# Kernel optimization log

Hardware: AMD Instinct MI355X
Metric: run time of the kernel (lower is better)

Reference implementation:

```python
import jax, jax.numpy as jnp
import numpy as np

B, T, C, H, E, K = 4, 2048, 512, 2048, 8, 2


def setup_inputs() -> dict:
    key = jax.random.key(0)
    ks = jax.random.split(key, 7)
    s_r = 1.0 / np.sqrt(C)
    s_h = 1.0 / np.sqrt(H)
    return {
        "x": jax.random.normal(ks[0], (B, T, C), dtype=jnp.float32),
        "Wr": jax.random.uniform(ks[1], (C, E), jnp.float32, -s_r, s_r),
        "br": jax.random.uniform(ks[2], (E,), jnp.float32, -s_r, s_r),
        "W1": jax.random.uniform(ks[3], (E, C, H), jnp.float32, -s_r, s_r),
        "b1": jax.random.uniform(ks[4], (E, H), jnp.float32, -s_r, s_r),
        "W2": jax.random.uniform(ks[5], (E, H, C), jnp.float32, -s_h, s_h),
        "b2": jax.random.uniform(ks[6], (E, C), jnp.float32, -s_h, s_h),
    }


def reference(x, Wr, br, W1, b1, W2, b2):
    # Router logits [B,T,E]
    logits = jnp.einsum("btc,ce->bte", x, Wr) + br
    topk_vals, topk_idx = jax.lax.top_k(logits, K)  # [B,T,K]
    scores = jax.nn.softmax(topk_vals, axis=-1)  # softmax over the K selected
    # Combine weights per expert: gate[b,t,e] = sum_k scores[b,t,k]*(idx==e)
    onehot = jax.nn.one_hot(topk_idx, E, dtype=x.dtype)  # [B,T,K,E]
    gate = jnp.einsum("btk,btke->bte", scores, onehot)  # [B,T,E]
    # Dense-masked expert MLPs (tokens not routed to e have gate==0)
    h = jax.nn.relu(jnp.einsum("btc,ech->bteh", x, W1) + b1)  # [B,T,E,H]
    y = jnp.einsum("bteh,ehc->btec", h, W2) + b2  # [B,T,E,C]
    out = jnp.einsum("btec,bte->btc", y, gate)  # weighted combine
    return logits, topk_idx, out
```

## Files before the change

### kernel.cpp

```cpp
#include <hip/hip_runtime.h>
#include <hip/hip_bf16.h>

#define NTOK 8192
#define NASN 16384
#define C_ 512
#define H_ 2048
#define E_ 8
#define NCH 128
#define CHTOK 64

typedef __bf16 bf16x8 __attribute__((ext_vector_type(8)));
typedef float f32x4 __attribute__((ext_vector_type(4)));

#define WS_COUNTS 0
#define WS_BASE   4096
#define WS_OFFS   8192
#define WS_T1S    8448
#define WS_INFO   8704
#define WS_TOKL   (WS_INFO + NTOK*16)
#define WS_SLOTS  (WS_TOKL + NASN*4)
#define WS_XBF    (WS_SLOTS + NTOK*8)
#define WS_W1B    (WS_XBF + (size_t)NTOK*C_*2)
#define WS_W2B    (WS_W1B + (size_t)E_*H_*C_*2)
#define WS_HS     (WS_W2B + (size_t)E_*H_*C_*2)
#define WS_YS     WS_XBF

__device__ __forceinline__ unsigned int f2bf(float f) {
  __hip_bfloat16 h = __float2bfloat16(f);
  return (unsigned int)*(unsigned short*)&h;
}
__device__ __forceinline__ float bf2f(unsigned int u) {
  return __int_as_float((u & 0xffffu) << 16);
}

__device__ __forceinline__ void g2l16(const unsigned short* g, unsigned short* l) {
  __builtin_amdgcn_global_load_lds(
      (const __attribute__((address_space(1))) unsigned int*)g,
      (__attribute__((address_space(3))) unsigned int*)l, 16, 0, 0);
}

__global__ __launch_bounds__(256) void k_router(
    const float* __restrict__ x, const float* __restrict__ Wr,
    const float* __restrict__ br, float* __restrict__ out_logits,
    float* __restrict__ out_idx, int4* __restrict__ info,
    int* __restrict__ counts, unsigned short* __restrict__ Xbf)
{
  int t = blockIdx.x * 4 + (threadIdx.x >> 6);
  int lane = threadIdx.x & 63;
  const float4* xr = (const float4*)(x + (size_t)t * C_);
  float4 x0 = xr[lane*2], x1 = xr[lane*2+1];
  uint4 pk;
  pk.x = f2bf(x0.x) | (f2bf(x0.y) << 16);
  pk.y = f2bf(x0.z) | (f2bf(x0.w) << 16);
  pk.z = f2bf(x1.x) | (f2bf(x1.y) << 16);
  pk.w = f2bf(x1.z) | (f2bf(x1.w) << 16);
  *(uint4*)(Xbf + (size_t)t * C_ + lane*8) = pk;

  float xs[8] = {x0.x,x0.y,x0.z,x0.w,x1.x,x1.y,x1.z,x1.w};
  float acc[8] = {0,0,0,0,0,0,0,0};
  #pragma unroll
  for (int j = 0; j < 8; j++) {
    const float4* w = (const float4*)(Wr + (size_t)(lane*8+j) * E_);
    float4 w0 = w[0], w1 = w[1];
    float we[8] = {w0.x,w0.y,w0.z,w0.w,w1.x,w1.y,w1.z,w1.w};
    #pragma unroll
    for (int e = 0; e < 8; e++) acc[e] += xs[j] * we[e];
  }
  #pragma unroll
  for (int off = 1; off < 64; off <<= 1) {
    #pragma unroll
    for (int e = 0; e < 8; e++) acc[e] += __shfl_xor(acc[e], off, 64);
  }
  #pragma unroll
  for (int e = 0; e < 8; e++) acc[e] += br[e];
  if (lane == 0) {
    #pragma unroll
    for (int e = 0; e < 8; e++) out_logits[t*8 + e] = acc[e];
    int i0 = 0; float v0 = acc[0];
    #pragma unroll
    for (int e = 1; e < 8; e++) if (acc[e] > v0) { v0 = acc[e]; i0 = e; }
    int i1 = -1; float v1 = -1e30f;
    #pragma unroll
    for (int e = 0; e < 8; e++) if (e != i0 && acc[e] > v1) { v1 = acc[e]; i1 = e; }
    float d = expf(v1 - v0);
    float s1 = d / (1.0f + d);
    float s0 = 1.0f - s1;
    out_idx[t*2]     = (float)i0;
    out_idx[t*2 + 1] = (float)i1;
    info[t] = make_int4(i0, i1, __float_as_int(s0), __float_as_int(s1));
    int ch = t >> 6;
    atomicAdd(&counts[ch*8 + i0], 1);
    atomicAdd(&counts[ch*8 + i1], 1);
  }
}

__global__ __launch_bounds__(256) void k_prefix(
    const int* __restrict__ counts, int* __restrict__ base,
    int* __restrict__ offs, int* __restrict__ t1s)
{
  __shared__ int lc[NCH*8];
  __shared__ int tot[8];
  __shared__ int off_s[9];
  int tid = threadIdx.x;
  for (int i = tid; i < NCH*8; i += 256) lc[i] = counts[i];
  __syncthreads();
  if (tid < 8) {
    int run = 0;
    for (int c = 0; c < NCH; c++) { int v = lc[c*8+tid]; lc[c*8+tid] = run; run += v; }
    tot[tid] = run;
  }
  __syncthreads();
  if (tid == 0) {
    int o = 0, t = 0;
    off_s[0] = 0; offs[0] = 0; t1s[0] = 0;
    for (int e = 0; e < 8; e++) {
      o += tot[e];
      off_s[e+1] = o; offs[e+1] = o;
      t += (tot[e] + 127) >> 7;
      t1s[e+1] = t;
    }
  }
  __syncthreads();
  for (int i = tid; i < NCH*8; i += 256) base[i] = off_s[i & 7] + lc[i];
}

__global__ __launch_bounds__(64) void k_scatter(
    const int4* __restrict__ info, const int* __restrict__ base,
    int* __restrict__ tokl, int2* __restrict__ slots2)
{
  __shared__ int cur[8];
  int c = blockIdx.x, tid = threadIdx.x;
  if (tid < 8) cur[tid] = base[c*8 + tid];
  __syncthreads();
  int t = c * CHTOK + tid;
  int4 nfo = info[t];
  int r0 = atomicAdd(&cur[nfo.x], 1);
  int r1 = atomicAdd(&cur[nfo.y], 1);
  tokl[r0] = t;
  tokl[r1] = t;
  slots2[t] = make_int2(r0, r1);
}

__global__ __launch_bounds__(256) void k_transpose(
    const float* __restrict__ in, unsigned short* __restrict__ outp, int R, int S)
{
  __shared__ float tile[128][33];
  size_t zo = (size_t)blockIdx.z * R * S;
  in += zo; outp += zo;
  int r0 = blockIdx.y * 128, s0 = blockIdx.x * 32;
  int t = threadIdx.x;
  #pragma unroll
  for (int i = 0; i < 16; i++) {
    int lin = i*256 + t;
    int rr = lin >> 5, ss = lin & 31;
    tile[rr][ss] = in[(size_t)(r0 + rr) * S + s0 + ss];
  }
  __syncthreads();
  #pragma unroll
  for (int i = 0; i < 4; i++) {
    int lin = i*256 + t;
    int ss = lin >> 5, rq = lin & 31;
    ushort4 v;
    v.x = (unsigned short)f2bf(tile[rq*4+0][ss]);
    v.y = (unsigned short)f2bf(tile[rq*4+1][ss]);
    v.z = (unsigned short)f2bf(tile[rq*4+2][ss]);
    v.w = (unsigned short)f2bf(tile[rq*4+3][ss]);
    *(ushort4*)(outp + (size_t)(s0 + ss) * R + r0 + rq*4) = v;
  }
}

__global__ __launch_bounds__(256) void k_gemm1(
    const unsigned short* __restrict__ Xbf, const int* __restrict__ tokl,
    const unsigned short* __restrict__ W1b,
    const float* __restrict__ b1, unsigned short* __restrict__ Hs,
    const int* __restrict__ offs, const int* __restrict__ t1s)
{
  __shared__ __align__(16) unsigned short AB[2*8192];
  int b = blockIdx.x;
  int mo = b >> 7, rr = b & 127;
  int n0 = (rr >> 3) * 128;
  int mt = mo*8 + (rr & 7);
  if (mt >= t1s[8]) return;
  int e = 0;
  #pragma unroll
  for (int i = 0; i < 7; i++) if (mt >= t1s[e+1]) e++;
  int row0 = offs[e] + (mt - t1s[e]) * 128;
  int rowEnd = offs[e+1];
  int tid = threadIdx.x, lane = tid & 63, w = tid >> 6;
  int wm = (w & 1) * 64, wn = (w >> 1) * 64;
  int quad = lane >> 4, l16 = lane & 15;
  const f32x4 zero = {0.f, 0.f, 0.f, 0.f};
  f32x4 acc[4][4];
  #pragma unroll
  for (int i = 0; i < 4; i++)
    #pragma unroll
    for (int j = 0; j < 4; j++) acc[i][j] = zero;
  const unsigned short* Bsrc = W1b + ((size_t)e * H_ + n0) * C_;

  const unsigned short* ga[2]; const unsigned short* gb[2];
  int lao[2], lbo[2];
  #pragma unroll
  for (int j = 0; j < 2; j++) {
    int L = (w*2 + j)*64 + lane;
    int row = L >> 2;
    int gc = (L & 3) ^ (row & 3);
    int gr = row0 + row; gr = gr < NASN-1 ? gr : NASN-1;
    int trow = tokl[gr];
    ga[j] = Xbf + (size_t)trow * C_ + gc*8;
    gb[j] = Bsrc + (size_t)row * C_ + gc*8;
    lao[j] = (w*2 + j)*512;
    lbo[j] = 4096 + (w*2 + j)*512;
  }
  int r3 = l16 & 3;
  const int KI = C_ / 32;

  #pragma unroll
  for (int j = 0; j < 2; j++) { g2l16(ga[j], AB + lao[j]); g2l16(gb[j], AB + lbo[j]); }

  for (int ki = 0; ki < KI; ki++) {
    int p = ki & 1;
    if (ki + 1 < KI) {
      int off = (ki + 1) * 32;
      unsigned short* nb = AB + (p ^ 1) * 8192;
      #pragma unroll
      for (int j = 0; j < 2; j++) {
        g2l16(ga[j] + off, nb + lao[j]);
        g2l16(gb[j] + off, nb + lbo[j]);
      }
      asm volatile("s_waitcnt vmcnt(4)" ::: "memory");
    } else {
      asm volatile("s_waitcnt vmcnt(0)" ::: "memory");
    }
    asm volatile("s_barrier" ::: "memory");

    const unsigned short* Ap = AB + p*8192;
    const unsigned short* Bp = Ap + 4096;
    int sl = (quad ^ r3) * 8;
    bf16x8 af[4], bfr[4];
    #pragma unroll
    for (int i = 0; i < 4; i++)
      af[i] = *(const bf16x8*)&Ap[(wm + i*16 + l16)*32 + sl];
    #pragma unroll
    for (int j = 0; j < 4; j++)
      bfr[j] = *(const bf16x8*)&Bp[(wn + j*16 + l16)*32 + sl];
    #pragma unroll
    for (int i = 0; i < 4; i++)
      #pragma unroll
      for (int j = 0; j < 4; j++)
        acc[i][j] = __builtin_amdgcn_mfma_f32_16x16x32_bf16(af[i], bfr[j], acc[i][j], 0, 0, 0);

    asm volatile("s_waitcnt lgkmcnt(0)" ::: "memory");
    asm volatile("s_barrier" ::: "memory");
  }

  unsigned short* Lt = AB + w*4096;
  #pragma unroll
  for (int j = 0; j < 4; j++) {
    int n = n0 + wn + j*16 + l16;
    float bias = b1[e * H_ + n];
    #pragma unroll
    for (int i = 0; i < 4; i++)
      #pragma unroll
      for (int r = 0; r < 4; r++) {
        float v = acc[i][j][r] + bias;
        Lt[(i*16 + quad*4 + r)*64 + j*16 + l16] = (unsigned short)f2bf(v > 0.f ? v : 0.f);
      }
  }
  #pragma unroll
  for (int it = 0; it < 8; it++) {
    int rloc = it*8 + (lane >> 3);
    int m = row0 + wm + rloc;
    uint4 vv = *(uint4*)&Lt[rloc*64 + (lane & 7)*8];
    if (m < rowEnd)
      *(uint4*)(Hs + (size_t)m * H_ + n0 + wn + (lane & 7)*8) = vv;
  }
}

__global__ __launch_bounds__(256) void k_gemm2(
    const unsigned short* __restrict__ Hs, const unsigned short* __restrict__ W2b,
    const float* __restrict__ b2, unsigned short* __restrict__ Ys,
    const int* __restrict__ offs, const int* __restrict__ t1s)
{
  __shared__ __align__(16) unsigned short AB[2*8192];
  int b = blockIdx.x;
  int g = b >> 5, rr = b & 31;
  int n0 = (rr >> 3) * 128;
  int mt = g*8 + (rr & 7);
  if (mt >= t1s[8]) return;
  int e = 0;
  #pragma unroll
  for (int i = 0; i < 7; i++) if (mt >= t1s[e+1]) e++;
  int row0 = offs[e] + (mt - t1s[e]) * 128;
  int rowEnd = offs[e+1];
  int tid = threadIdx.x, lane = tid & 63, w = tid >> 6;
  int wm = (w & 1) * 64, wn = (w >> 1) * 64;
  int quad = lane >> 4, l16 = lane & 15;
  const f32x4 zero = {0.f, 0.f, 0.f, 0.f};
  f32x4 acc[4][4];
  #pragma unroll
  for (int i = 0; i < 4; i++)
    #pragma unroll
    for (int j = 0; j < 4; j++) acc[i][j] = zero;
  const unsigned short* Bsrc = W2b + ((size_t)e * C_ + n0) * H_;

  const unsigned short* ga[2]; const unsigned short* gb[2];
  int lao[2], lbo[2];
  #pragma unroll
  for (int j = 0; j < 2; j++) {
    int L = (w*2 + j)*64 + lane;
    int row = L >> 2;
    int gc = (L & 3) ^ (row & 3);
    int gr = row0 + row; gr = gr < NASN-1 ? gr : NASN-1;
    ga[j] = Hs + (size_t)gr * H_ + gc*8;
    gb[j] = Bsrc + (size_t)row * H_ + gc*8;
    lao[j] = (w*2 + j)*512;
    lbo[j] = 4096 + (w*2 + j)*512;
  }
  int r3 = l16 & 3;
  const int KI = H_ / 32;

  #pragma unroll
  for (int j = 0; j < 2; j++) { g2l16(ga[j], AB + lao[j]); g2l16(gb[j], AB + lbo[j]); }

  for (int ki = 0; ki < KI; ki++) {
    int p = ki & 1;
    if (ki + 1 < KI) {
      int off = (ki + 1) * 32;
      unsigned short* nb = AB + (p ^ 1) * 8192;
      #pragma unroll
      for (int j = 0; j < 2; j++) {
        g2l16(ga[j] + off, nb + lao[j]);
        g2l16(gb[j] + off, nb + lbo[j]);
      }
      asm volatile("s_waitcnt vmcnt(4)" ::: "memory");
    } else {
      asm volatile("s_waitcnt vmcnt(0)" ::: "memory");
    }
    asm volatile("s_barrier" ::: "memory");

    const unsigned short* Ap = AB + p*8192;
    const unsigned short* Bp = Ap + 4096;
    int sl = (quad ^ r3) * 8;
    bf16x8 af[4], bfr[4];
    #pragma unroll
    for (int i = 0; i < 4; i++)
      af[i] = *(const bf16x8*)&Ap[(wm + i*16 + l16)*32 + sl];
    #pragma unroll
    for (int j = 0; j < 4; j++)
      bfr[j] = *(const bf16x8*)&Bp[(wn + j*16 + l16)*32 + sl];
    #pragma unroll
    for (int i = 0; i < 4; i++)
      #pragma unroll
      for (int j = 0; j < 4; j++)
        acc[i][j] = __builtin_amdgcn_mfma_f32_16x16x32_bf16(af[i], bfr[j], acc[i][j], 0, 0, 0);

    asm volatile("s_waitcnt lgkmcnt(0)" ::: "memory");
    asm volatile("s_barrier" ::: "memory");
  }

  unsigned short* Lt = AB + w*4096;
  #pragma unroll
  for (int j = 0; j < 4; j++) {
    int n = n0 + wn + j*16 + l16;
    float bias = b2[e * C_ + n];
    #pragma unroll
    for (int i = 0; i < 4; i++)
      #pragma unroll
      for (int r = 0; r < 4; r++)
        Lt[(i*16 + quad*4 + r)*64 + j*16 + l16] =
            (unsigned short)f2bf(acc[i][j][r] + bias);
  }
  #pragma unroll
  for (int it = 0; it < 8; it++) {
    int rloc = it*8 + (lane >> 3);
    int m = row0 + wm + rloc;
    uint4 vv = *(uint4*)&Lt[rloc*64 + (lane & 7)*8];
    if (m < rowEnd)
      *(uint4*)(Ys + (size_t)m * C_ + n0 + wn + (lane & 7)*8) = vv;
  }
}

__global__ __launch_bounds__(256) void k_combine(
    const unsigned short* __restrict__ Ys, const int4* __restrict__ info,
    const int2* __restrict__ slots2, float* __restrict__ outp)
{
  int t = blockIdx.x * 4 + (threadIdx.x >> 6);
  int lane = threadIdx.x & 63;
  int4 nfo = info[t];
  int2 ss = slots2[t];
  float g0 = __int_as_float(nfo.z), g1 = __int_as_float(nfo.w);
  uint4 a = *(const uint4*)(Ys + (size_t)ss.x * C_ + lane*8);
  uint4 bb = *(const uint4*)(Ys + (size_t)ss.y * C_ + lane*8);
  unsigned int au[4] = {a.x, a.y, a.z, a.w};
  unsigned int bu[4] = {bb.x, bb.y, bb.z, bb.w};
  float vals[8];
  #pragma unroll
  for (int q = 0; q < 4; q++) {
    vals[q*2]   = g0*bf2f(au[q])       + g1*bf2f(bu[q]);
    vals[q*2+1] = g0*bf2f(au[q] >> 16) + g1*bf2f(bu[q] >> 16);
  }
  float4 o0, o1;
  o0.x = vals[0]; o0.y = vals[1]; o0.z = vals[2]; o0.w = vals[3];
  o1.x = vals[4]; o1.y = vals[5]; o1.z = vals[6]; o1.w = vals[7];
  float4* o = (float4*)(outp + (size_t)t * C_ + lane*8);
  o[0] = o0;
  o[1] = o1;
}

extern "C" void kernel_launch(void* const* d_in, const int* in_sizes, int n_in,
                              void* d_out, int out_size, void* d_ws, size_t ws_size,
                              hipStream_t stream)
{
  const float* x  = (const float*)d_in[0];
  const float* Wr = (const float*)d_in[1];
  const float* br = (const float*)d_in[2];
  const float* W1 = (const float*)d_in[3];
  const float* b1 = (const float*)d_in[4];
  const float* W2 = (const float*)d_in[5];
  const float* b2 = (const float*)d_in[6];
  float* out = (float*)d_out;
  char* ws = (char*)d_ws;

  int*  counts = (int*)(ws + WS_COUNTS);
  int*  base   = (int*)(ws + WS_BASE);
  int*  offs   = (int*)(ws + WS_OFFS);
  int*  t1s    = (int*)(ws + WS_T1S);
  int4* info   = (int4*)(ws + WS_INFO);
  int*  tokl   = (int*)(ws + WS_TOKL);
  int2* slots2 = (int2*)(ws + WS_SLOTS);
  unsigned short* Xbf = (unsigned short*)(ws + WS_XBF);
  unsigned short* W1b = (unsigned short*)(ws + WS_W1B);
  unsigned short* W2b = (unsigned short*)(ws + WS_W2B);
  unsigned short* Hs  = (unsigned short*)(ws + WS_HS);
  unsigned short* Ys  = (unsigned short*)(ws + WS_YS);

  hipMemsetAsync(counts, 0, NCH*8*sizeof(int), stream);

  k_transpose<<<dim3(H_/32, C_/128, E_), 256, 0, stream>>>(W1, W1b, C_, H_);
  k_transpose<<<dim3(C_/32, H_/128, E_), 256, 0, stream>>>(W2, W2b, H_, C_);
  k_router<<<NTOK/4, 256, 0, stream>>>(x, Wr, br, out, out + 65536, info, counts, Xbf);
  k_prefix<<<1, 256, 0, stream>>>(counts, base, offs, t1s);
  k_scatter<<<NCH, 64, 0, stream>>>(info, base, tokl, slots2);
  k_gemm1<<<17*128, 256, 0, stream>>>(Xbf, tokl, W1b, b1, Hs, offs, t1s);
  k_gemm2<<<17*32, 256, 0, stream>>>(Hs, W2b, b2, Ys, offs, t1s);
  k_combine<<<NTOK/4, 256, 0, stream>>>(Ys, info, slots2, out + 81920);
}
```

Before: 279.6 us.

## Halve gemm2 M-tile to 64 rows and change LDS swizzle layout for both GEMMs

The second expert GEMM now uses 64-row M tiles instead of 128, with a separate tile-prefix array (t2s) and about twice as many blocks. The intent is better CU occupancy and load balance for the small N=512 output, where gemm2 previously launched only about 544 blocks. Both GEMMs also switch to a new LDS staging layout that pairs two rows per 64-element line with an XOR swizzle, meant to reduce LDS bank conflicts on fragment reads. The smaller tile lowers data reuse per block and re-reads W2 more often.

```diff
diff --git a/kernel.cpp b/kernel.cpp
--- a/kernel.cpp
+++ b/kernel.cpp
@@ -16,7 +16,8 @@
 #define WS_BASE   4096
 #define WS_OFFS   8192
 #define WS_T1S    8448
-#define WS_INFO   8704
+#define WS_T2S    8704
+#define WS_INFO   8960
 #define WS_TOKL   (WS_INFO + NTOK*16)
 #define WS_SLOTS  (WS_TOKL + NASN*4)
 #define WS_XBF    (WS_SLOTS + NTOK*8)
@@ -37,6 +38,13 @@
   __builtin_amdgcn_global_load_lds(
       (const __attribute__((address_space(1))) unsigned int*)g,
       (__attribute__((address_space(3))) unsigned int*)l, 16, 0, 0);
+}
+
+__device__ __forceinline__ void stage_decode(int L, int& brow, int& q) {
+  int s = L >> 3, slot = L & 7;
+  int v = slot ^ (s & 7);
+  brow = 2*s + (v >> 2);
+  q = v & 3;
 }
 
 __global__ __launch_bounds__(256) void k_router(
@@ -96,7 +104,7 @@
 
 __global__ __launch_bounds__(256) void k_prefix(
     const int* __restrict__ counts, int* __restrict__ base,
-    int* __restrict__ offs, int* __restrict__ t1s)
+    int* __restrict__ offs, int* __restrict__ t1s, int* __restrict__ t2s)
 {
   __shared__ int lc[NCH*8];
   __shared__ int tot[8];
@@ -111,13 +119,15 @@
   }
   __syncthreads();
   if (tid == 0) {
-    int o = 0, t = 0;
-    off_s[0] = 0; offs[0] = 0; t1s[0] = 0;
+    int o = 0, t1 = 0, t2 = 0;
+    off_s[0] = 0; offs[0] = 0; t1s[0] = 0; t2s[0] = 0;
     for (int e = 0; e < 8; e++) {
       o += tot[e];
       off_s[e+1] = o; offs[e+1] = o;
-      t += (tot[e] + 127) >> 7;
-      t1s[e+1] = t;
+      t1 += (tot[e] + 127) >> 7;
+      t1s[e+1] = t1;
+      t2 += (tot[e] + 63) >> 6;
+      t2s[e+1] = t2;
     }
   }
   __syncthreads();
@@ -202,16 +212,15 @@
   #pragma unroll
   for (int j = 0; j < 2; j++) {
     int L = (w*2 + j)*64 + lane;
-    int row = L >> 2;
-    int gc = (L & 3) ^ (row & 3);
-    int gr = row0 + row; gr = gr < NASN-1 ? gr : NASN-1;
+    int brow, q; stage_decode(L, brow, q);
+    int gr = row0 + brow; gr = gr < NASN-1 ? gr : NASN-1;
     int trow = tokl[gr];
-    ga[j] = Xbf + (size_t)trow * C_ + gc*8;
-    gb[j] = Bsrc + (size_t)row * C_ + gc*8;
+    ga[j] = Xbf + (size_t)trow * C_ + q*8;
+    gb[j] = Bsrc + (size_t)brow * C_ + q*8;
     lao[j] = (w*2 + j)*512;
     lbo[j] = 4096 + (w*2 + j)*512;
   }
-  int r3 = l16 & 3;
+  int rbase = (l16>>1)*64 + ((((l16&1)<<2) + quad) ^ (l16>>1))*8;
   const int KI = C_ / 32;
 
   #pragma unroll
@@ -235,14 +244,13 @@
 
     const unsigned short* Ap = AB + p*8192;
     const unsigned short* Bp = Ap + 4096;
-    int sl = (quad ^ r3) * 8;
     bf16x8 af[4], bfr[4];
     #pragma unroll
     for (int i = 0; i < 4; i++)
-      af[i] = *(const bf16x8*)&Ap[(wm + i*16 + l16)*32 + sl];
+      af[i] = *(const bf16x8*)&Ap[wm*32 + i*512 + rbase];
     #pragma unroll
     for (int j = 0; j < 4; j++)
-      bfr[j] = *(const bf16x8*)&Bp[(wn + j*16 + l16)*32 + sl];
+      bfr[j] = *(const bf16x8*)&Bp[wn*32 + j*512 + rbase];
     #pragma unroll
     for (int i = 0; i < 4; i++)
       #pragma unroll
@@ -279,77 +287,78 @@
 __global__ __launch_bounds__(256) void k_gemm2(
     const unsigned short* __restrict__ Hs, const unsigned short* __restrict__ W2b,
     const float* __restrict__ b2, unsigned short* __restrict__ Ys,
-    const int* __restrict__ offs, const int* __restrict__ t1s)
-{
-  __shared__ __align__(16) unsigned short AB[2*8192];
+    const int* __restrict__ offs, const int* __restrict__ t2s)
+{
+  __shared__ __align__(16) unsigned short AB[2*6144];
   int b = blockIdx.x;
-  int g = b >> 5, rr = b & 31;
+  int mo = b >> 5, rr = b & 31;
   int n0 = (rr >> 3) * 128;
-  int mt = g*8 + (rr & 7);
-  if (mt >= t1s[8]) return;
+  int mt = mo*8 + (rr & 7);
+  if (mt >= t2s[8]) return;
   int e = 0;
   #pragma unroll
-  for (int i = 0; i < 7; i++) if (mt >= t1s[e+1]) e++;
-  int row0 = offs[e] + (mt - t1s[e]) * 128;
+  for (int i = 0; i < 7; i++) if (mt >= t2s[e+1]) e++;
+  int row0 = offs[e] + (mt - t2s[e]) * 64;
   int rowEnd = offs[e+1];
   int tid = threadIdx.x, lane = tid & 63, w = tid >> 6;
-  int wm = (w & 1) * 64, wn = (w >> 1) * 64;
+  int wm = (w & 1) * 32, wn = (w >> 1) * 64;
   int quad = lane >> 4, l16 = lane & 15;
   const f32x4 zero = {0.f, 0.f, 0.f, 0.f};
-  f32x4 acc[4][4];
-  #pragma unroll
-  for (int i = 0; i < 4; i++)
+  f32x4 acc[2][4];
+  #pragma unroll
+  for (int i = 0; i < 2; i++)
     #pragma unroll
     for (int j = 0; j < 4; j++) acc[i][j] = zero;
   const unsigned short* Bsrc = W2b + ((size_t)e * C_ + n0) * H_;
 
-  const unsigned short* ga[2]; const unsigned short* gb[2];
-  int lao[2], lbo[2];
+  const unsigned short* gA; int laoA;
+  const unsigned short* gb[2]; int lbo[2];
+  {
+    int L = w*64 + lane;
+    int brow, q; stage_decode(L, brow, q);
+    int gr = row0 + brow; gr = gr < NASN-1 ? gr : NASN-1;
+    gA = Hs + (size_t)gr * H_ + q*8;
+    laoA = w*512;
+  }
   #pragma unroll
   for (int j = 0; j < 2; j++) {
     int L = (w*2 + j)*64 + lane;
-    int row = L >> 2;
-    int gc = (L & 3) ^ (row & 3);
-    int gr = row0 + row; gr = gr < NASN-1 ? gr : NASN-1;
-    ga[j] = Hs + (size_t)gr * H_ + gc*8;
-    gb[j] = Bsrc + (size_t)row * H_ + gc*8;
-    lao[j] = (w*2 + j)*512;
-    lbo[j] = 4096 + (w*2 + j)*512;
-  }
-  int r3 = l16 & 3;
+    int brow, q; stage_decode(L, brow, q);
+    gb[j] = Bsrc + (size_t)brow * H_ + q*8;
+    lbo[j] = 2048 + (w*2 + j)*512;
+  }
+  int rbase = (l16>>1)*64 + ((((l16&1)<<2) + quad) ^ (l16>>1))*8;
   const int KI = H_ / 32;
 
-  #pragma unroll
-  for (int j = 0; j < 2; j++) { g2l16(ga[j], AB + lao[j]); g2l16(gb[j], AB + lbo[j]); }
+  g2l16(gA, AB + laoA);
+  #pragma unroll
+  for (int j = 0; j < 2; j++) g2l16(gb[j], AB + lbo[j]);
 
   for (int ki = 0; ki < KI; ki++) {
     int p = ki & 1;
     if (ki + 1 < KI) {
       int off = (ki + 1) * 32;
-      unsigned short* nb = AB + (p ^ 1) * 8192;
-      #pragma unroll
-      for (int j = 0; j < 2; j++) {
-        g2l16(ga[j] + off, nb + lao[j]);
-        g2l16(gb[j] + off, nb + lbo[j]);
-      }
-      asm volatile("s_waitcnt vmcnt(4)" ::: "memory");
+      unsigned short* nb = AB + (p ^ 1) * 6144;
+      g2l16(gA + off, nb + laoA);
+      #pragma unroll
+      for (int j = 0; j < 2; j++) g2l16(gb[j] + off, nb + lbo[j]);
+      asm volatile("s_waitcnt vmcnt(3)" ::: "memory");
     } else {
       asm volatile("s_waitcnt vmcnt(0)" ::: "memory");
     }
     asm volatile("s_barrier" ::: "memory");
 
-    const unsigned short* Ap = AB + p*8192;
-    const unsigned short* Bp = Ap + 4096;
-    int sl = (quad ^ r3) * 8;
-    bf16x8 af[4], bfr[4];
-    #pragma unroll
-    for (int i = 0; i < 4; i++)
-      af[i] = *(const bf16x8*)&Ap[(wm + i*16 + l16)*32 + sl];
+    const unsigned short* Ap = AB + p*6144;
+    const unsigned short* Bp = Ap + 2048;
+    bf16x8 af[2], bfr[4];
+    #pragma unroll
+    for (int i = 0; i < 2; i++)
+      af[i] = *(const bf16x8*)&Ap[wm*32 + i*512 + rbase];
     #pragma unroll
     for (int j = 0; j < 4; j++)
-      bfr[j] = *(const bf16x8*)&Bp[(wn + j*16 + l16)*32 + sl];
-    #pragma unroll
-    for (int i = 0; i < 4; i++)
+      bfr[j] = *(const bf16x8*)&Bp[wn*32 + j*512 + rbase];
+    #pragma unroll
+    for (int i = 0; i < 2; i++)
       #pragma unroll
       for (int j = 0; j < 4; j++)
         acc[i][j] = __builtin_amdgcn_mfma_f32_16x16x32_bf16(af[i], bfr[j], acc[i][j], 0, 0, 0);
@@ -358,20 +367,20 @@
     asm volatile("s_barrier" ::: "memory");
   }
 
-  unsigned short* Lt = AB + w*4096;
+  unsigned short* Lt = AB + w*2048;
   #pragma unroll
   for (int j = 0; j < 4; j++) {
     int n = n0 + wn + j*16 + l16;
     float bias = b2[e * C_ + n];
     #pragma unroll
-    for (int i = 0; i < 4; i++)
+    for (int i = 0; i < 2; i++)
       #pragma unroll
       for (int r = 0; r < 4; r++)
         Lt[(i*16 + quad*4 + r)*64 + j*16 + l16] =
             (unsigned short)f2bf(acc[i][j][r] + bias);
   }
   #pragma unroll
-  for (int it = 0; it < 8; it++) {
+  for (int it = 0; it < 4; it++) {
     int rloc = it*8 + (lane >> 3);
     int m = row0 + wm + rloc;
     uint4 vv = *(uint4*)&Lt[rloc*64 + (lane & 7)*8];
@@ -425,6 +434,7 @@
   int*  base   = (int*)(ws + WS_BASE);
   int*  offs   = (int*)(ws + WS_OFFS);
   int*  t1s    = (int*)(ws + WS_T1S);
+  int*  t2s    = (int*)(ws + WS_T2S);
   int4* info   = (int4*)(ws + WS_INFO);
   int*  tokl   = (int*)(ws + WS_TOKL);
   int2* slots2 = (int2*)(ws + WS_SLOTS);
@@ -439,9 +449,9 @@
   k_transpose<<<dim3(H_/32, C_/128, E_), 256, 0, stream>>>(W1, W1b, C_, H_);
   k_transpose<<<dim3(C_/32, H_/128, E_), 256, 0, stream>>>(W2, W2b, H_, C_);
   k_router<<<NTOK/4, 256, 0, stream>>>(x, Wr, br, out, out + 65536, info, counts, Xbf);
-  k_prefix<<<1, 256, 0, stream>>>(counts, base, offs, t1s);
+  k_prefix<<<1, 256, 0, stream>>>(counts, base, offs, t1s, t2s);
   k_scatter<<<NCH, 64, 0, stream>>>(info, base, tokl, slots2);
   k_gemm1<<<17*128, 256, 0, stream>>>(Xbf, tokl, W1b, b1, Hs, offs, t1s);
-  k_gemm2<<<17*32, 256, 0, stream>>>(Hs, W2b, b2, Ys, offs, t1s);
+  k_gemm2<<<33*32, 256, 0, stream>>>(Hs, W2b, b2, Ys, offs, t2s);
   k_combine<<<NTOK/4, 256, 0, stream>>>(Ys, info, slots2, out + 81920);
 }
```

After: 285.4 us. 2.1% more time.

## Fuse router with weight transposes, merge prefix into scatter, rework LDS swizzle

Applied to the files above, without the earlier changes.

Router and both weight-transpose kernels now run as one launch, partitioned by block index. Per-block expert counts are written with plain stores instead of global atomics, which removes the memset. Prefix and scatter are merged so each scatter block recomputes its own base offsets from the per-block counts. This cuts four launches and a memset down to two. The GEMM staging layout also changes to an 8-slot XOR swizzle over pairs of rows, meant to reduce LDS bank conflicts on fragment reads. The cost is that every scatter block re-reads all 16K count entries.

```diff
diff --git a/kernel.cpp b/kernel.cpp
--- a/kernel.cpp
+++ b/kernel.cpp
@@ -6,17 +6,15 @@
 #define C_ 512
 #define H_ 2048
 #define E_ 8
-#define NCH 128
-#define CHTOK 64
+#define RBC 2048
 
 typedef __bf16 bf16x8 __attribute__((ext_vector_type(8)));
 typedef float f32x4 __attribute__((ext_vector_type(4)));
 
 #define WS_COUNTS 0
-#define WS_BASE   4096
-#define WS_OFFS   8192
-#define WS_T1S    8448
-#define WS_INFO   8704
+#define WS_OFFS   65536
+#define WS_T1S    65792
+#define WS_INFO   66048
 #define WS_TOKL   (WS_INFO + NTOK*16)
 #define WS_SLOTS  (WS_TOKL + NASN*4)
 #define WS_XBF    (WS_SLOTS + NTOK*8)
@@ -39,134 +37,173 @@
       (__attribute__((address_space(3))) unsigned int*)l, 16, 0, 0);
 }
 
-__global__ __launch_bounds__(256) void k_router(
+__device__ __forceinline__ void stage_decode(int L, int& brow, int& q) {
+  int s = L >> 3, slot = L & 7;
+  int v = slot ^ (s & 7);
+  brow = 2*s + (v >> 2);
+  q = v & 3;
+}
+
+__global__ __launch_bounds__(256) void k_fused(
     const float* __restrict__ x, const float* __restrict__ Wr,
     const float* __restrict__ br, float* __restrict__ out_logits,
     float* __restrict__ out_idx, int4* __restrict__ info,
-    int* __restrict__ counts, unsigned short* __restrict__ Xbf)
-{
-  int t = blockIdx.x * 4 + (threadIdx.x >> 6);
-  int lane = threadIdx.x & 63;
-  const float4* xr = (const float4*)(x + (size_t)t * C_);
-  float4 x0 = xr[lane*2], x1 = xr[lane*2+1];
-  uint4 pk;
-  pk.x = f2bf(x0.x) | (f2bf(x0.y) << 16);
-  pk.y = f2bf(x0.z) | (f2bf(x0.w) << 16);
-  pk.z = f2bf(x1.x) | (f2bf(x1.y) << 16);
-  pk.w = f2bf(x1.z) | (f2bf(x1.w) << 16);
-  *(uint4*)(Xbf + (size_t)t * C_ + lane*8) = pk;
-
-  float xs[8] = {x0.x,x0.y,x0.z,x0.w,x1.x,x1.y,x1.z,x1.w};
-  float acc[8] = {0,0,0,0,0,0,0,0};
-  #pragma unroll
-  for (int j = 0; j < 8; j++) {
-    const float4* w = (const float4*)(Wr + (size_t)(lane*8+j) * E_);
-    float4 w0 = w[0], w1 = w[1];
-    float we[8] = {w0.x,w0.y,w0.z,w0.w,w1.x,w1.y,w1.z,w1.w};
-    #pragma unroll
-    for (int e = 0; e < 8; e++) acc[e] += xs[j] * we[e];
-  }
-  #pragma unroll
-  for (int off = 1; off < 64; off <<= 1) {
-    #pragma unroll
-    for (int e = 0; e < 8; e++) acc[e] += __shfl_xor(acc[e], off, 64);
-  }
-  #pragma unroll
-  for (int e = 0; e < 8; e++) acc[e] += br[e];
-  if (lane == 0) {
-    #pragma unroll
-    for (int e = 0; e < 8; e++) out_logits[t*8 + e] = acc[e];
-    int i0 = 0; float v0 = acc[0];
-    #pragma unroll
-    for (int e = 1; e < 8; e++) if (acc[e] > v0) { v0 = acc[e]; i0 = e; }
-    int i1 = -1; float v1 = -1e30f;
-    #pragma unroll
-    for (int e = 0; e < 8; e++) if (e != i0 && acc[e] > v1) { v1 = acc[e]; i1 = e; }
-    float d = expf(v1 - v0);
-    float s1 = d / (1.0f + d);
-    float s0 = 1.0f - s1;
-    out_idx[t*2]     = (float)i0;
-    out_idx[t*2 + 1] = (float)i1;
-    info[t] = make_int4(i0, i1, __float_as_int(s0), __float_as_int(s1));
-    int ch = t >> 6;
-    atomicAdd(&counts[ch*8 + i0], 1);
-    atomicAdd(&counts[ch*8 + i1], 1);
-  }
-}
-
-__global__ __launch_bounds__(256) void k_prefix(
-    const int* __restrict__ counts, int* __restrict__ base,
+    int* __restrict__ counts, unsigned short* __restrict__ Xbf,
+    const float* __restrict__ W1, unsigned short* __restrict__ W1b,
+    const float* __restrict__ W2, unsigned short* __restrict__ W2b)
+{
+  __shared__ float tileS[128][33];
+  __shared__ int bc[8];
+  int b = blockIdx.x;
+  int tid = threadIdx.x;
+
+  if (b < RBC) {
+    if (tid < 8) bc[tid] = 0;
+    __syncthreads();
+    int t = b * 4 + (tid >> 6);
+    int lane = tid & 63;
+    const float4* xr = (const float4*)(x + (size_t)t * C_);
+    float4 x0 = xr[lane*2], x1 = xr[lane*2+1];
+    uint4 pk;
+    pk.x = f2bf(x0.x) | (f2bf(x0.y) << 16);
+    pk.y = f2bf(x0.z) | (f2bf(x0.w) << 16);
+    pk.z = f2bf(x1.x) | (f2bf(x1.y) << 16);
+    pk.w = f2bf(x1.z) | (f2bf(x1.w) << 16);
+    *(uint4*)(Xbf + (size_t)t * C_ + lane*8) = pk;
+
+    float xs[8] = {x0.x,x0.y,x0.z,x0.w,x1.x,x1.y,x1.z,x1.w};
+    float acc[8] = {0,0,0,0,0,0,0,0};
+    #pragma unroll
+    for (int j = 0; j < 8; j++) {
+      const float4* w = (const float4*)(Wr + (size_t)(lane*8+j) * E_);
+      float4 w0 = w[0], w1 = w[1];
+      float we[8] = {w0.x,w0.y,w0.z,w0.w,w1.x,w1.y,w1.z,w1.w};
+      #pragma unroll
+      for (int e = 0; e < 8; e++) acc[e] += xs[j] * we[e];
+    }
+    #pragma unroll
+    for (int off = 1; off < 64; off <<= 1) {
+      #pragma unroll
+      for (int e = 0; e < 8; e++) acc[e] += __shfl_xor(acc[e], off, 64);
+    }
+    #pragma unroll
+    for (int e = 0; e < 8; e++) acc[e] += br[e];
+    if (lane == 0) {
+      #pragma unroll
+      for (int e = 0; e < 8; e++) out_logits[t*8 + e] = acc[e];
+      int i0 = 0; float v0 = acc[0];
+      #pragma unroll
+      for (int e = 1; e < 8; e++) if (acc[e] > v0) { v0 = acc[e]; i0 = e; }
+      int i1 = -1; float v1 = -1e30f;
+      #pragma unroll
+      for (int e = 0; e < 8; e++) if (e != i0 && acc[e] > v1) { v1 = acc[e]; i1 = e; }
+      float d = expf(v1 - v0);
+      float s1 = d / (1.0f + d);
+      float s0 = 1.0f - s1;
+      out_idx[t*2]     = (float)i0;
+      out_idx[t*2 + 1] = (float)i1;
+      info[t] = make_int4(i0, i1, __float_as_int(s0), __float_as_int(s1));
+      atomicAdd(&bc[i0], 1);
+      atomicAdd(&bc[i1], 1);
+    }
+    __syncthreads();
+    if (tid < 8) counts[b*8 + tid] = bc[tid];
+    return;
+  }
+
+  const float* in; unsigned short* outp; int R, S, bx, by, bz;
+  if (b < 2*RBC) {
+    int bb = b - RBC;
+    in = W1; outp = W1b; R = C_; S = H_;
+    bx = bb & 63; by = (bb >> 6) & 3; bz = bb >> 8;
+  } else {
+    int bb = b - 2*RBC;
+    in = W2; outp = W2b; R = H_; S = C_;
+    bx = bb & 15; by = (bb >> 4) & 15; bz = bb >> 8;
+  }
+  size_t zo = (size_t)bz * R * S;
+  in += zo; outp += zo;
+  int r0 = by * 128, s0 = bx * 32;
+  #pragma unroll
+  for (int i = 0; i < 16; i++) {
+    int lin = i*256 + tid;
+    int rr = lin >> 5, ss = lin & 31;
+    tileS[rr][ss] = in[(size_t)(r0 + rr) * S + s0 + ss];
+  }
+  __syncthreads();
+  #pragma unroll
+  for (int i = 0; i < 4; i++) {
+    int lin = i*256 + tid;
+    int ss = lin >> 5, rq = lin & 31;
+    ushort4 v;
+    v.x = (unsigned short)f2bf(tileS[rq*4+0][ss]);
+    v.y = (unsigned short)f2bf(tileS[rq*4+1][ss]);
+    v.z = (unsigned short)f2bf(tileS[rq*4+2][ss]);
+    v.w = (unsigned short)f2bf(tileS[rq*4+3][ss]);
+    *(ushort4*)(outp + (size_t)(s0 + ss) * R + r0 + rq*4) = v;
+  }
+}
+
+__global__ __launch_bounds__(64) void k_prefscatter(
+    const int* __restrict__ counts, const int4* __restrict__ info,
+    int* __restrict__ tokl, int2* __restrict__ slots2,
     int* __restrict__ offs, int* __restrict__ t1s)
 {
-  __shared__ int lc[NCH*8];
-  __shared__ int tot[8];
+  __shared__ int full_s[8][8];
+  __shared__ int part_s[8][8];
+  __shared__ int tot_s[8];
   __shared__ int off_s[9];
-  int tid = threadIdx.x;
-  for (int i = tid; i < NCH*8; i += 256) lc[i] = counts[i];
+  __shared__ int cur[8];
+  int c = blockIdx.x, t = threadIdx.x;
+  int e = t & 7, g = t >> 3;
+  int lim = c * 16;
+  int full = 0, part = 0;
+  for (int i = 0; i < 256; i++) {
+    int rb = g*256 + i;
+    int v = counts[rb*8 + e];
+    full += v;
+    if (rb < lim) part += v;
+  }
+  full_s[e][g] = full; part_s[e][g] = part;
   __syncthreads();
-  if (tid < 8) {
-    int run = 0;
-    for (int c = 0; c < NCH; c++) { int v = lc[c*8+tid]; lc[c*8+tid] = run; run += v; }
-    tot[tid] = run;
+  if (t < 8) {
+    int s = 0;
+    #pragma unroll
+    for (int gg = 0; gg < 8; gg++) s += full_s[t][gg];
+    tot_s[t] = s;
   }
   __syncthreads();
-  if (tid == 0) {
-    int o = 0, t = 0;
-    off_s[0] = 0; offs[0] = 0; t1s[0] = 0;
-    for (int e = 0; e < 8; e++) {
-      o += tot[e];
-      off_s[e+1] = o; offs[e+1] = o;
-      t += (tot[e] + 127) >> 7;
-      t1s[e+1] = t;
+  if (t == 0) {
+    int o = 0;
+    off_s[0] = 0;
+    for (int ee = 0; ee < 8; ee++) { o += tot_s[ee]; off_s[ee+1] = o; }
+    if (c == 0) {
+      offs[0] = 0; t1s[0] = 0;
+      int tt = 0;
+      for (int ee = 0; ee < 8; ee++) {
+        offs[ee+1] = off_s[ee+1];
+        tt += (tot_s[ee] + 127) >> 7;
+        t1s[ee+1] = tt;
+      }
     }
   }
   __syncthreads();
-  for (int i = tid; i < NCH*8; i += 256) base[i] = off_s[i & 7] + lc[i];
-}
-
-__global__ __launch_bounds__(64) void k_scatter(
-    const int4* __restrict__ info, const int* __restrict__ base,
-    int* __restrict__ tokl, int2* __restrict__ slots2)
-{
-  __shared__ int cur[8];
-  int c = blockIdx.x, tid = threadIdx.x;
-  if (tid < 8) cur[tid] = base[c*8 + tid];
+  if (t < 8) {
+    int mg = c >> 4;
+    int bse = off_s[t];
+    #pragma unroll
+    for (int gg = 0; gg < 8; gg++) if (gg < mg) bse += full_s[t][gg];
+    bse += part_s[t][mg];
+    cur[t] = bse;
+  }
   __syncthreads();
-  int t = c * CHTOK + tid;
-  int4 nfo = info[t];
+  int tok = c*64 + t;
+  int4 nfo = info[tok];
   int r0 = atomicAdd(&cur[nfo.x], 1);
   int r1 = atomicAdd(&cur[nfo.y], 1);
-  tokl[r0] = t;
-  tokl[r1] = t;
-  slots2[t] = make_int2(r0, r1);
-}
-
-__global__ __launch_bounds__(256) void k_transpose(
-    const float* __restrict__ in, unsigned short* __restrict__ outp, int R, int S)
-{
-  __shared__ float tile[128][33];
-  size_t zo = (size_t)blockIdx.z * R * S;
-  in += zo; outp += zo;
-  int r0 = blockIdx.y * 128, s0 = blockIdx.x * 32;
-  int t = threadIdx.x;
-  #pragma unroll
-  for (int i = 0; i < 16; i++) {
-    int lin = i*256 + t;
-    int rr = lin >> 5, ss = lin & 31;
-    tile[rr][ss] = in[(size_t)(r0 + rr) * S + s0 + ss];
-  }
-  __syncthreads();
-  #pragma unroll
-  for (int i = 0; i < 4; i++) {
-    int lin = i*256 + t;
-    int ss = lin >> 5, rq = lin & 31;
-    ushort4 v;
-    v.x = (unsigned short)f2bf(tile[rq*4+0][ss]);
-    v.y = (unsigned short)f2bf(tile[rq*4+1][ss]);
-    v.z = (unsigned short)f2bf(tile[rq*4+2][ss]);
-    v.w = (unsigned short)f2bf(tile[rq*4+3][ss]);
-    *(ushort4*)(outp + (size_t)(s0 + ss) * R + r0 + rq*4) = v;
-  }
+  tokl[r0] = tok;
+  tokl[r1] = tok;
+  slots2[tok] = make_int2(r0, r1);
 }
 
 __global__ __launch_bounds__(256) void k_gemm1(
@@ -202,16 +239,15 @@
   #pragma unroll
   for (int j = 0; j < 2; j++) {
     int L = (w*2 + j)*64 + lane;
-    int row = L >> 2;
-    int gc = (L & 3) ^ (row & 3);
-    int gr = row0 + row; gr = gr < NASN-1 ? gr : NASN-1;
+    int brow, q; stage_decode(L, brow, q);
+    int gr = row0 + brow; gr = gr < NASN-1 ? gr : NASN-1;
     int trow = tokl[gr];
-    ga[j] = Xbf + (size_t)trow * C_ + gc*8;
-    gb[j] = Bsrc + (size_t)row * C_ + gc*8;
+    ga[j] = Xbf + (size_t)trow * C_ + q*8;
+    gb[j] = Bsrc + (size_t)brow * C_ + q*8;
     lao[j] = (w*2 + j)*512;
     lbo[j] = 4096 + (w*2 + j)*512;
   }
-  int r3 = l16 & 3;
+  int rbase = (l16>>1)*64 + ((((l16&1)<<2) + quad) ^ (l16>>1))*8;
   const int KI = C_ / 32;
 
   #pragma unroll
@@ -235,14 +271,13 @@
 
     const unsigned short* Ap = AB + p*8192;
     const unsigned short* Bp = Ap + 4096;
-    int sl = (quad ^ r3) * 8;
     bf16x8 af[4], bfr[4];
     #pragma unroll
     for (int i = 0; i < 4; i++)
-      af[i] = *(const bf16x8*)&Ap[(wm + i*16 + l16)*32 + sl];
+      af[i] = *(const bf16x8*)&Ap[wm*32 + i*512 + rbase];
     #pragma unroll
     for (int j = 0; j < 4; j++)
-      bfr[j] = *(const bf16x8*)&Bp[(wn + j*16 + l16)*32 + sl];
+      bfr[j] = *(const bf16x8*)&Bp[wn*32 + j*512 + rbase];
     #pragma unroll
     for (int i = 0; i < 4; i++)
       #pragma unroll
@@ -283,9 +318,9 @@
 {
   __shared__ __align__(16) unsigned short AB[2*8192];
   int b = blockIdx.x;
-  int g = b >> 5, rr = b & 31;
+  int mo = b >> 5, rr = b & 31;
   int n0 = (rr >> 3) * 128;
-  int mt = g*8 + (rr & 7);
+  int mt = mo*8 + (rr & 7);
   if (mt >= t1s[8]) return;
   int e = 0;
   #pragma unroll
@@ -308,15 +343,14 @@
   #pragma unroll
   for (int j = 0; j < 2; j++) {
     int L = (w*2 + j)*64 + lane;
-    int row = L >> 2;
-    int gc = (L & 3) ^ (row & 3);
-    int gr = row0 + row; gr = gr < NASN-1 ? gr : NASN-1;
-    ga[j] = Hs + (size_t)gr * H_ + gc*8;
-    gb[j] = Bsrc + (size_t)row * H_ + gc*8;
+    int brow, q; stage_decode(L, brow, q);
+    int gr = row0 + brow; gr = gr < NASN-1 ? gr : NASN-1;
+    ga[j] = Hs + (size_t)gr * H_ + q*8;
+    gb[j] = Bsrc + (size_t)brow * H_ + q*8;
     lao[j] = (w*2 + j)*512;
     lbo[j] = 4096 + (w*2 + j)*512;
   }
-  int r3 = l16 & 3;
+  int rbase = (l16>>1)*64 + ((((l16&1)<<2) + quad) ^ (l16>>1))*8;
   const int KI = H_ / 32;
 
   #pragma unroll
@@ -340,14 +374,13 @@
 
     const unsigned short* Ap = AB + p*8192;
     const unsigned short* Bp = Ap + 4096;
-    int sl = (quad ^ r3) * 8;
     bf16x8 af[4], bfr[4];
     #pragma unroll
     for (int i = 0; i < 4; i++)
-      af[i] = *(const bf16x8*)&Ap[(wm + i*16 + l16)*32 + sl];
+      af[i] = *(const bf16x8*)&Ap[wm*32 + i*512 + rbase];
     #pragma unroll
     for (int j = 0; j < 4; j++)
-      bfr[j] = *(const bf16x8*)&Bp[(wn + j*16 + l16)*32 + sl];
+      bfr[j] = *(const bf16x8*)&Bp[wn*32 + j*512 + rbase];
     #pragma unroll
     for (int i = 0; i < 4; i++)
       #pragma unroll
@@ -422,7 +455,6 @@
   char* ws = (char*)d_ws;
 
   int*  counts = (int*)(ws + WS_COUNTS);
-  int*  base   = (int*)(ws + WS_BASE);
   int*  offs   = (int*)(ws + WS_OFFS);
   int*  t1s    = (int*)(ws + WS_T1S);
   int4* info   = (int4*)(ws + WS_INFO);
@@ -434,13 +466,9 @@
   unsigned short* Hs  = (unsigned short*)(ws + WS_HS);
   unsigned short* Ys  = (unsigned short*)(ws + WS_YS);
 
-  hipMemsetAsync(counts, 0, NCH*8*sizeof(int), stream);
-
-  k_transpose<<<dim3(H_/32, C_/128, E_), 256, 0, stream>>>(W1, W1b, C_, H_);
-  k_transpose<<<dim3(C_/32, H_/128, E_), 256, 0, stream>>>(W2, W2b, H_, C_);
-  k_router<<<NTOK/4, 256, 0, stream>>>(x, Wr, br, out, out + 65536, info, counts, Xbf);
-  k_prefix<<<1, 256, 0, stream>>>(counts, base, offs, t1s);
-  k_scatter<<<NCH, 64, 0, stream>>>(info, base, tokl, slots2);
+  k_fused<<<3*RBC, 256, 0, stream>>>(x, Wr, br, out, out + 65536, info,
+                                     counts, Xbf, W1, W1b, W2, W2b);
+  k_prefscatter<<<128, 64, 0, stream>>>(counts, info, tokl, slots2, offs, t1s);
   k_gemm1<<<17*128, 256, 0, stream>>>(Xbf, tokl, W1b, b1, Hs, offs, t1s);
   k_gemm2<<<17*32, 256, 0, stream>>>(Hs, W2b, b2, Ys, offs, t1s);
   k_combine<<<NTOK/4, 256, 0, stream>>>(Ys, info, slots2, out + 81920);
```

Measured after the change: 272.5 us. -2.5%, faster.
